# Kernel tuning notes

Measured on AMD Instinct MI355X. Metric: run time of the kernel, lower is better.

Reference implementation:

```python
import jax, jax.numpy as jnp
import numpy as np

N_POINTS = 100000
N_PAIRS = 50000   # pairs per kernel offset
K_OFFSETS = 27    # 3^3 kernel offsets for 3D kernel_size=3
C = 128


def setup_inputs() -> dict:
    key = jax.random.key(0)
    ks = jax.random.split(key, 7)
    features = jax.random.normal(ks[0], (N_POINTS, C), dtype=jnp.float32)
    in_map = jax.random.randint(ks[1], (K_OFFSETS, N_PAIRS), 0, N_POINTS)
    out_map = jax.random.randint(ks[2], (K_OFFSETS, N_PAIRS), 0, N_POINTS)
    # scale weights so two stacked convs stay numerically tame in fp32
    W0 = jax.random.normal(ks[3], (K_OFFSETS, C, C), dtype=jnp.float32) * 0.05
    b0 = jax.random.normal(ks[4], (C,), dtype=jnp.float32)
    W1 = jax.random.normal(ks[5], (K_OFFSETS, C, C), dtype=jnp.float32) * 0.05
    b1 = jax.random.normal(ks[6], (C,), dtype=jnp.float32)
    return {"features": features, "in_map": in_map, "out_map": out_map,
            "W0": W0, "b0": b0, "W1": W1, "b1": b1}


def _sparse_conv(x, W, b, in_map, out_map, n_out):
    """Minkowski-style sparse conv: gather -> per-offset matmul -> scatter-add.
    x: [N, C], W: [K, C, C], in_map/out_map: [K, P]."""
    gathered = x[in_map]                                  # [K, P, C]
    msg = jnp.einsum('kpc,kcd->kpd', gathered, W)         # [K, P, C]
    y = jax.ops.segment_sum(msg.reshape(-1, msg.shape[-1]),
                            out_map.reshape(-1),
                            num_segments=n_out)           # [N, C]
    return y + b


def reference(features, in_map, out_map, W0, b0, W1, b1):
    n = features.shape[0]
    out = jax.nn.relu(_sparse_conv(features, W0, b0, in_map, out_map, n))
    out = _sparse_conv(out, W1, b1, in_map, out_map, n)
    return out + features
```

## Files before the change

kernel.cpp:

```cpp
#include <hip/hip_runtime.h>

#define N_POINTS 100000
#define N_PAIRS  50000
#define K_OFFSETS 27
#define C 128
#define WPAD 136
#define CAP 48

#define CSR_GROUPS 8
#define CSR_BPG 128

typedef __attribute__((ext_vector_type(8))) short short8;
typedef __attribute__((ext_vector_type(4))) float floatx4;

__device__ inline unsigned short f2bf(float f) {
  unsigned int u = __float_as_uint(f);
  return (unsigned short)((u + 0x7FFFu + ((u >> 16) & 1u)) >> 16);
}
__device__ inline float bf2f(unsigned int lo16) {
  return __uint_as_float(lo16 << 16);
}

__global__ __launch_bounds__(256) void prep_w_kernel(
    const float* __restrict__ W0, const float* __restrict__ W1,
    unsigned short* __restrict__ WT0, unsigned short* __restrict__ WT1) {
  int i = blockIdx.x * 256 + threadIdx.x;
  const int per = K_OFFSETS * C * C;
  if (i >= 2 * per) return;
  const float* W = (i < per) ? W0 : W1;
  unsigned short* WT = (i < per) ? WT0 : WT1;
  int r = (i < per) ? i : i - per;
  int k = r / (C * C);
  int q = r % (C * C);
  int d = q / C;
  int c = q % C;
  WT[k * C * C + d * C + c] = f2bf(W[k * C * C + c * C + d]);
}

__global__ __launch_bounds__(256) void prep_x_kernel(
    const float* __restrict__ features, const float* __restrict__ b0,
    unsigned short* __restrict__ xb, float* __restrict__ out, int write_out) {
  int i = (blockIdx.x * 256 + threadIdx.x) * 4;
  if (i >= N_POINTS * C) return;
  float4 f = *(const float4*)&features[i];
  ushort4 u;
  u.x = f2bf(f.x); u.y = f2bf(f.y); u.z = f2bf(f.z); u.w = f2bf(f.w);
  *(ushort4*)&xb[i] = u;
  if (write_out) {
    float4 b = *(const float4*)&b0[i & 127];
    *(float4*)&out[i] = b;
  }
}

__global__ __launch_bounds__(256) void zero_counts_kernel(int* __restrict__ counts) {
  int i = blockIdx.x * 256 + threadIdx.x;
  if (i < N_POINTS) counts[i] = 0;
}

__global__ __launch_bounds__(256) void build_csr_kernel(
    const int* __restrict__ out_map, int* __restrict__ counts, int* __restrict__ idxbuf) {
  const int grp = blockIdx.x & (CSR_GROUPS - 1);
  const int blk = blockIdx.x >> 3;
  const int lo = grp * (N_POINTS / CSR_GROUPS);
  const int hi = lo + (N_POINTS / CSR_GROUPS);
  const int total4 = K_OFFSETS * N_PAIRS / 4;
  for (int i4 = blk * 256 + (int)threadIdx.x; i4 < total4; i4 += CSR_BPG * 256) {
    int4 o4 = *(const int4*)&out_map[i4 * 4];
    int o[4] = {o4.x, o4.y, o4.z, o4.w};
#pragma unroll
    for (int j = 0; j < 4; ++j) {
      if (o[j] >= lo && o[j] < hi) {
        int pos = atomicAdd(&counts[o[j]], 1);
        int flat = i4 * 4 + j;
        int k = flat / N_PAIRS;
        int p = flat - k * N_PAIRS;
        if (pos < CAP) idxbuf[o[j] * CAP + pos] = (k << 16) | p;
      }
    }
  }
}

__global__ __launch_bounds__(256, 4) void conv_msg_kernel(
    const unsigned short* __restrict__ xb, const unsigned short* __restrict__ wbt,
    const int* __restrict__ in_map, unsigned short* __restrict__ msg, int k0) {
  __shared__ unsigned short Wlds[C * WPAD];

  const int k = k0 + blockIdx.y;
  const int pairBase = blockIdx.x * 128;
  const int tid = threadIdx.x;

  const unsigned short* wk = wbt + k * C * C;
#pragma unroll
  for (int it = 0; it < 8; ++it) {
    int t = tid + it * 256;
    int row = t >> 4;
    int col = (t & 15) << 3;
    *(uint4*)&Wlds[row * WPAD + col] = *(const uint4*)&wk[row * C + col];
  }
  __syncthreads();

  const int wave = tid >> 6;
  const int lane = tid & 63;
  const int l15 = lane & 15;
  const int kg = lane >> 4;
  const int pair0 = pairBase + wave * 32;

  const int prA0 = pair0 + l15;
  const int prA1 = pair0 + 16 + l15;
  const int inIdx0 = (prA0 < N_PAIRS) ? in_map[k * N_PAIRS + prA0] : 0;
  const int inIdx1 = (prA1 < N_PAIRS) ? in_map[k * N_PAIRS + prA1] : 0;
  const unsigned short* arow0 = xb + (size_t)inIdx0 * C + kg * 8;
  const unsigned short* arow1 = xb + (size_t)inIdx1 * C + kg * 8;

  floatx4 acc0[8], acc1[8];
#pragma unroll
  for (int nt = 0; nt < 8; ++nt) {
    acc0[nt] = (floatx4){0.f, 0.f, 0.f, 0.f};
    acc1[nt] = (floatx4){0.f, 0.f, 0.f, 0.f};
  }

#pragma unroll
  for (int kk = 0; kk < 4; ++kk) {
    short8 a0 = *(const short8*)(arow0 + kk * 32);
    short8 a1 = *(const short8*)(arow1 + kk * 32);
    const unsigned short* bbase = &Wlds[l15 * WPAD + kk * 32 + kg * 8];
#pragma unroll
    for (int nt = 0; nt < 8; ++nt) {
      short8 b = *(const short8*)(bbase + nt * 16 * WPAD);
      acc0[nt] = __builtin_amdgcn_mfma_f32_16x16x32_bf16(a0, b, acc0[nt], 0, 0, 0);
      acc1[nt] = __builtin_amdgcn_mfma_f32_16x16x32_bf16(a1, b, acc1[nt], 0, 0, 0);
    }
  }

#pragma unroll
  for (int i = 0; i < 4; ++i) {
    int pr0 = pair0 + kg * 4 + i;
    if (pr0 < N_PAIRS) {
      unsigned short* row = msg + (size_t)(blockIdx.y * N_PAIRS + pr0) * C;
      uint4 v;
      v.x = (unsigned int)f2bf(acc0[0][i]) | ((unsigned int)f2bf(acc0[1][i]) << 16);
      v.y = (unsigned int)f2bf(acc0[2][i]) | ((unsigned int)f2bf(acc0[3][i]) << 16);
      v.z = (unsigned int)f2bf(acc0[4][i]) | ((unsigned int)f2bf(acc0[5][i]) << 16);
      v.w = (unsigned int)f2bf(acc0[6][i]) | ((unsigned int)f2bf(acc0[7][i]) << 16);
      *(uint4*)(row + l15 * 8) = v;
    }
    int pr1 = pair0 + 16 + kg * 4 + i;
    if (pr1 < N_PAIRS) {
      unsigned short* row = msg + (size_t)(blockIdx.y * N_PAIRS + pr1) * C;
      uint4 v;
      v.x = (unsigned int)f2bf(acc1[0][i]) | ((unsigned int)f2bf(acc1[1][i]) << 16);
      v.y = (unsigned int)f2bf(acc1[2][i]) | ((unsigned int)f2bf(acc1[3][i]) << 16);
      v.z = (unsigned int)f2bf(acc1[4][i]) | ((unsigned int)f2bf(acc1[5][i]) << 16);
      v.w = (unsigned int)f2bf(acc1[6][i]) | ((unsigned int)f2bf(acc1[7][i]) << 16);
      *(uint4*)(row + l15 * 8) = v;
    }
  }
}

__global__ __launch_bounds__(256) void gather_kernel(
    const unsigned short* __restrict__ msg, const int* __restrict__ counts,
    const int* __restrict__ idxbuf, const float* __restrict__ bias,
    const float* __restrict__ features, float* __restrict__ out,
    unsigned short* __restrict__ x1b,
    int k0, int G, int init_mode, int fin_mode) {
  __shared__ int elds[4][64];
  const int wave = threadIdx.x >> 6;
  const int lane = threadIdx.x & 63;
  const int oi = blockIdx.x * 4 + wave;

  const int c0 = ((2 * lane) & 7) * 16 + (lane >> 2);
  const int c1 = c0 + 16;
  const size_t base = (size_t)oi * C;

  float a0, a1;
  if (init_mode == 1)      { a0 = bias[c0]; a1 = bias[c1]; }
  else if (init_mode == 2) { a0 = bias[c0] + features[base + c0];
                             a1 = bias[c1] + features[base + c1]; }
  else                     { a0 = out[base + c0]; a1 = out[base + c1]; }

  int cnt = counts[oi]; if (cnt > CAP) cnt = CAP;

  int e_mine = (lane < cnt) ? idxbuf[oi * CAP + lane] : 0;
  bool ok = false;
  if (lane < cnt) {
    unsigned int rel = ((unsigned int)e_mine >> 16) - (unsigned int)k0;
    ok = rel < (unsigned int)G;
  }
  unsigned long long mask = __ballot(ok);
  int cnt2 = __popcll(mask);
  if (ok) {
    int pos = __popcll(mask & ((1ull << lane) - 1ull));
    unsigned int rel = ((unsigned int)e_mine >> 16) - (unsigned int)k0;
    elds[wave][pos] = (int)(rel * N_PAIRS + ((unsigned int)e_mine & 0xffffu));
  }
  __syncthreads();

  const unsigned short* mbase = msg + 2 * lane;
  int t = 0;
  for (; t + 4 <= cnt2; t += 4) {
    int f0 = elds[wave][t];
    int f1 = elds[wave][t + 1];
    int f2 = elds[wave][t + 2];
    int f3 = elds[wave][t + 3];
    unsigned int v0 = *(const unsigned int*)(mbase + (size_t)f0 * C);
    unsigned int v1 = *(const unsigned int*)(mbase + (size_t)f1 * C);
    unsigned int v2 = *(const unsigned int*)(mbase + (size_t)f2 * C);
    unsigned int v3 = *(const unsigned int*)(mbase + (size_t)f3 * C);
    a0 += bf2f(v0 & 0xffffu) + bf2f(v1 & 0xffffu) + bf2f(v2 & 0xffffu) + bf2f(v3 & 0xffffu);
    a1 += bf2f(v0 >> 16) + bf2f(v1 >> 16) + bf2f(v2 >> 16) + bf2f(v3 >> 16);
  }
  for (; t < cnt2; ++t) {
    int f0 = elds[wave][t];
    unsigned int v = *(const unsigned int*)(mbase + (size_t)f0 * C);
    a0 += bf2f(v & 0xffffu);
    a1 += bf2f(v >> 16);
  }

  if (fin_mode == 1) {
    x1b[base + c0] = f2bf(fmaxf(a0, 0.f));
    x1b[base + c1] = f2bf(fmaxf(a1, 0.f));
  } else {
    out[base + c0] = a0;
    out[base + c1] = a1;
  }
}

__global__ __launch_bounds__(256) void mid_kernel(
    const float* __restrict__ features, const float* __restrict__ b1,
    float* __restrict__ out, unsigned short* __restrict__ x1b) {
  int i = (blockIdx.x * 256 + threadIdx.x) * 4;
  if (i >= N_POINTS * C) return;
  float4 y = *(const float4*)&out[i];
  ushort4 u;
  u.x = f2bf(fmaxf(y.x, 0.f));
  u.y = f2bf(fmaxf(y.y, 0.f));
  u.z = f2bf(fmaxf(y.z, 0.f));
  u.w = f2bf(fmaxf(y.w, 0.f));
  *(ushort4*)&x1b[i] = u;
  float4 f = *(const float4*)&features[i];
  float4 b = *(const float4*)&b1[i & 127];
  float4 o;
  o.x = f.x + b.x; o.y = f.y + b.y; o.z = f.z + b.z; o.w = f.w + b.w;
  *(float4*)&out[i] = o;
}

__global__ __launch_bounds__(256, 4) void conv_atomic_kernel(
    const unsigned short* __restrict__ xb, const unsigned short* __restrict__ wbt,
    const int* __restrict__ in_map, const int* __restrict__ out_map,
    float* __restrict__ out) {
  __shared__ unsigned short Wlds[C * WPAD];
  const int k = blockIdx.y;
  const int pairBase = blockIdx.x * 64;
  const int tid = threadIdx.x;
  const unsigned short* wk = wbt + k * C * C;
#pragma unroll
  for (int it = 0; it < 8; ++it) {
    int t = tid + it * 256;
    int row = t >> 4;
    int col = (t & 15) << 3;
    *(uint4*)&Wlds[row * WPAD + col] = *(const uint4*)&wk[row * C + col];
  }
  __syncthreads();
  const int wave = tid >> 6;
  const int lane = tid & 63;
  const int l15 = lane & 15;
  const int kg = lane >> 4;
  const int pair0 = pairBase + wave * 16;
  const int prA = pair0 + l15;
  const int inIdx = (prA < N_PAIRS) ? in_map[k * N_PAIRS + prA] : 0;
  const unsigned short* arow = xb + (size_t)inIdx * C + kg * 8;
  floatx4 acc[8];
#pragma unroll
  for (int nt = 0; nt < 8; ++nt) acc[nt] = (floatx4){0.f, 0.f, 0.f, 0.f};
#pragma unroll
  for (int kk = 0; kk < 4; ++kk) {
    short8 a = *(const short8*)(arow + kk * 32);
    const unsigned short* bbase = &Wlds[l15 * WPAD + kk * 32 + kg * 8];
#pragma unroll
    for (int nt = 0; nt < 8; ++nt) {
      short8 b = *(const short8*)(bbase + nt * 16 * WPAD);
      acc[nt] = __builtin_amdgcn_mfma_f32_16x16x32_bf16(a, b, acc[nt], 0, 0, 0);
    }
  }
#pragma unroll
  for (int i = 0; i < 4; ++i) {
    int pr = pair0 + kg * 4 + i;
    if (pr < N_PAIRS) {
      int oi = out_map[k * N_PAIRS + pr];
      float* orow = out + (size_t)oi * C + l15;
#pragma unroll
      for (int nt = 0; nt < 8; ++nt) atomicAdd(orow + nt * 16, acc[nt][i]);
    }
  }
}

extern "C" void kernel_launch(void* const* d_in, const int* in_sizes, int n_in,
                              void* d_out, int out_size, void* d_ws, size_t ws_size,
                              hipStream_t stream) {
  const float* features = (const float*)d_in[0];
  const int* in_map     = (const int*)d_in[1];
  const int* out_map    = (const int*)d_in[2];
  const float* W0       = (const float*)d_in[3];
  const float* b0       = (const float*)d_in[4];
  const float* W1       = (const float*)d_in[5];
  const float* b1       = (const float*)d_in[6];
  float* out = (float*)d_out;

  char* ws = (char*)d_ws;
  unsigned short* xb  = (unsigned short*)(ws);
  unsigned short* x1b = (unsigned short*)(ws + 25600000);
  unsigned short* WT0 = (unsigned short*)(ws + 51200000);
  unsigned short* WT1 = (unsigned short*)(ws + 52084736);
  int* counts         = (int*)(ws + 52969472);
  int* idxbuf         = (int*)(ws + 53369856);
  unsigned short* msg = (unsigned short*)(ws + 72569856);

  const long long MSG_K_BYTES = (long long)N_PAIRS * C * 2;
  long long avail = (long long)ws_size - 72569856LL;
  int G = 0;
  if (avail >= MSG_K_BYTES) {
    long long g = avail / MSG_K_BYTES;
    G = (int)(g > K_OFFSETS ? K_OFFSETS : g);
  }

  prep_w_kernel<<<(2 * K_OFFSETS * C * C + 255) / 256, 256, 0, stream>>>(W0, W1, WT0, WT1);
  prep_x_kernel<<<(N_POINTS * C / 4 + 255) / 256, 256, 0, stream>>>(
      features, b0, xb, out, (G > 0) ? 0 : 1);

  if (G > 0) {
    zero_counts_kernel<<<(N_POINTS + 255) / 256, 256, 0, stream>>>(counts);
    build_csr_kernel<<<CSR_GROUPS * CSR_BPG, 256, 0, stream>>>(out_map, counts, idxbuf);

    const int nchunks = (K_OFFSETS + G - 1) / G;
    for (int layer = 0; layer < 2; ++layer) {
      const unsigned short* xin = layer ? x1b : xb;
      const unsigned short* wt  = layer ? WT1 : WT0;
      const float* bias         = layer ? b1  : b0;
      for (int c = 0; c < nchunks; ++c) {
        int k0 = c * G;
        int Gc = K_OFFSETS - k0 < G ? K_OFFSETS - k0 : G;
        dim3 cgrid((N_PAIRS + 127) / 128, Gc);
        conv_msg_kernel<<<cgrid, 256, 0, stream>>>(xin, wt, in_map, msg, k0);
        int init_mode = (c == 0) ? (layer ? 2 : 1) : 0;
        int fin_mode  = (layer == 0 && c == nchunks - 1) ? 1 : 0;
        gather_kernel<<<N_POINTS / 4, 256, 0, stream>>>(
            msg, counts, idxbuf, bias, features, out, x1b, k0, Gc, init_mode, fin_mode);
      }
    }
  } else {
    dim3 cgrid((N_PAIRS + 63) / 64, K_OFFSETS);
    conv_atomic_kernel<<<cgrid, 256, 0, stream>>>(xb, WT0, in_map, out_map, out);
    mid_kernel<<<(N_POINTS * C / 4 + 255) / 256, 256, 0, stream>>>(features, b1, out, x1b);
    conv_atomic_kernel<<<cgrid, 256, 0, stream>>>(x1b, WT1, in_map, out_map, out);
  }
}
```

Baseline: 672.7 us.

## Write messages into per-output CSR slots so gather reads contiguous rows

Replaces the capped per-output index list with a counting pass plus prefix-sum allocation per chunk. The conv kernel now claims a slot by atomic cursor and writes each message row directly into the output point's contiguous segment. The gather then streams consecutive rows without index lookups, LDS compaction or a barrier. This removes the CAP truncation but adds an atomic and an out_map read per pair row in the conv kernel, and the scattered writes may hurt store coalescing.

```diff
diff --git a/kernel.cpp b/kernel.cpp
--- a/kernel.cpp
+++ b/kernel.cpp
@@ -5,7 +5,8 @@
 #define K_OFFSETS 27
 #define C 128
 #define WPAD 136
-#define CAP 48
+
+#define NCH_MAX 7
 
 #define CSR_GROUPS 8
 #define CSR_BPG 128
@@ -52,13 +53,15 @@
   }
 }
 
-__global__ __launch_bounds__(256) void zero_counts_kernel(int* __restrict__ counts) {
+__global__ __launch_bounds__(256) void zero_meta_kernel(
+    int* __restrict__ countc, int* __restrict__ ccur) {
   int i = blockIdx.x * 256 + threadIdx.x;
-  if (i < N_POINTS) counts[i] = 0;
-}
-
-__global__ __launch_bounds__(256) void build_csr_kernel(
-    const int* __restrict__ out_map, int* __restrict__ counts, int* __restrict__ idxbuf) {
+  if (i < NCH_MAX * N_POINTS) countc[i] = 0;
+  if (i < NCH_MAX) ccur[i] = 0;
+}
+
+__global__ __launch_bounds__(256) void count_kernel(
+    const int* __restrict__ out_map, int* __restrict__ countc, int PG) {
   const int grp = blockIdx.x & (CSR_GROUPS - 1);
   const int blk = blockIdx.x >> 3;
   const int lo = grp * (N_POINTS / CSR_GROUPS);
@@ -70,19 +73,42 @@
 #pragma unroll
     for (int j = 0; j < 4; ++j) {
       if (o[j] >= lo && o[j] < hi) {
-        int pos = atomicAdd(&counts[o[j]], 1);
-        int flat = i4 * 4 + j;
-        int k = flat / N_PAIRS;
-        int p = flat - k * N_PAIRS;
-        if (pos < CAP) idxbuf[o[j] * CAP + pos] = (k << 16) | p;
+        int c = (i4 * 4 + j) / PG;
+        atomicAdd(&countc[c * N_POINTS + o[j]], 1);
       }
     }
   }
 }
 
-__global__ __launch_bounds__(256, 4) void conv_msg_kernel(
+__global__ __launch_bounds__(256) void alloc_kernel(
+    const int* __restrict__ countc, int* __restrict__ startc,
+    int* __restrict__ cursA, int* __restrict__ cursB, int* __restrict__ ccur) {
+  const int c = blockIdx.y;
+  const int oi = blockIdx.x * 256 + (int)threadIdx.x;
+  const int lane = threadIdx.x & 63;
+  int cnt = (oi < N_POINTS) ? countc[c * N_POINTS + oi] : 0;
+  int x = cnt;
+#pragma unroll
+  for (int off = 1; off < 64; off <<= 1) {
+    int y = __shfl_up(x, off);
+    if (lane >= off) x += y;
+  }
+  int wtot = __shfl(x, 63);
+  int base = 0;
+  if (lane == 63) base = atomicAdd(&ccur[c], wtot);
+  base = __shfl(base, 63);
+  int s = base + x - cnt;
+  if (oi < N_POINTS) {
+    startc[c * N_POINTS + oi] = s;
+    cursA[c * N_POINTS + oi] = s;
+    cursB[c * N_POINTS + oi] = s;
+  }
+}
+
+__global__ __launch_bounds__(256, 4) void conv_msg_csr_kernel(
     const unsigned short* __restrict__ xb, const unsigned short* __restrict__ wbt,
-    const int* __restrict__ in_map, unsigned short* __restrict__ msg, int k0) {
+    const int* __restrict__ in_map, const int* __restrict__ out_map,
+    int* __restrict__ curs, unsigned short* __restrict__ msg2, int k0) {
   __shared__ unsigned short Wlds[C * WPAD];
 
   const int k = k0 + blockIdx.y;
@@ -136,7 +162,11 @@
   for (int i = 0; i < 4; ++i) {
     int pr0 = pair0 + kg * 4 + i;
     if (pr0 < N_PAIRS) {
-      unsigned short* row = msg + (size_t)(blockIdx.y * N_PAIRS + pr0) * C;
+      int o = out_map[k * N_PAIRS + pr0];
+      int sl = 0;
+      if (l15 == 0) sl = atomicAdd(&curs[o], 1);
+      sl = __shfl(sl, kg * 16);
+      unsigned short* row = msg2 + (size_t)sl * C;
       uint4 v;
       v.x = (unsigned int)f2bf(acc0[0][i]) | ((unsigned int)f2bf(acc0[1][i]) << 16);
       v.y = (unsigned int)f2bf(acc0[2][i]) | ((unsigned int)f2bf(acc0[3][i]) << 16);
@@ -146,7 +176,11 @@
     }
     int pr1 = pair0 + 16 + kg * 4 + i;
     if (pr1 < N_PAIRS) {
-      unsigned short* row = msg + (size_t)(blockIdx.y * N_PAIRS + pr1) * C;
+      int o = out_map[k * N_PAIRS + pr1];
+      int sl = 0;
+      if (l15 == 0) sl = atomicAdd(&curs[o], 1);
+      sl = __shfl(sl, kg * 16);
+      unsigned short* row = msg2 + (size_t)sl * C;
       uint4 v;
       v.x = (unsigned int)f2bf(acc1[0][i]) | ((unsigned int)f2bf(acc1[1][i]) << 16);
       v.y = (unsigned int)f2bf(acc1[2][i]) | ((unsigned int)f2bf(acc1[3][i]) << 16);
@@ -157,13 +191,11 @@
   }
 }
 
-__global__ __launch_bounds__(256) void gather_kernel(
-    const unsigned short* __restrict__ msg, const int* __restrict__ counts,
-    const int* __restrict__ idxbuf, const float* __restrict__ bias,
+__global__ __launch_bounds__(256) void gather_csr_kernel(
+    const unsigned short* __restrict__ msg2, const int* __restrict__ countc,
+    const int* __restrict__ startc, const float* __restrict__ bias,
     const float* __restrict__ features, float* __restrict__ out,
-    unsigned short* __restrict__ x1b,
-    int k0, int G, int init_mode, int fin_mode) {
-  __shared__ int elds[4][64];
+    unsigned short* __restrict__ x1b, int init_mode, int fin_mode) {
   const int wave = threadIdx.x >> 6;
   const int lane = threadIdx.x & 63;
   const int oi = blockIdx.x * 4 + wave;
@@ -178,40 +210,21 @@
                              a1 = bias[c1] + features[base + c1]; }
   else                     { a0 = out[base + c0]; a1 = out[base + c1]; }
 
-  int cnt = counts[oi]; if (cnt > CAP) cnt = CAP;
-
-  int e_mine = (lane < cnt) ? idxbuf[oi * CAP + lane] : 0;
-  bool ok = false;
-  if (lane < cnt) {
-    unsigned int rel = ((unsigned int)e_mine >> 16) - (unsigned int)k0;
-    ok = rel < (unsigned int)G;
-  }
-  unsigned long long mask = __ballot(ok);
-  int cnt2 = __popcll(mask);
-  if (ok) {
-    int pos = __popcll(mask & ((1ull << lane) - 1ull));
-    unsigned int rel = ((unsigned int)e_mine >> 16) - (unsigned int)k0;
-    elds[wave][pos] = (int)(rel * N_PAIRS + ((unsigned int)e_mine & 0xffffu));
-  }
-  __syncthreads();
-
-  const unsigned short* mbase = msg + 2 * lane;
+  const int cnt = countc[oi];
+  const int s0 = startc[oi];
+  const unsigned short* mb = msg2 + (size_t)s0 * C + 2 * lane;
+
   int t = 0;
-  for (; t + 4 <= cnt2; t += 4) {
-    int f0 = elds[wave][t];
-    int f1 = elds[wave][t + 1];
-    int f2 = elds[wave][t + 2];
-    int f3 = elds[wave][t + 3];
-    unsigned int v0 = *(const unsigned int*)(mbase + (size_t)f0 * C);
-    unsigned int v1 = *(const unsigned int*)(mbase + (size_t)f1 * C);
-    unsigned int v2 = *(const unsigned int*)(mbase + (size_t)f2 * C);
-    unsigned int v3 = *(const unsigned int*)(mbase + (size_t)f3 * C);
+  for (; t + 4 <= cnt; t += 4) {
+    unsigned int v0 = *(const unsigned int*)(mb + (t + 0) * C);
+    unsigned int v1 = *(const unsigned int*)(mb + (t + 1) * C);
+    unsigned int v2 = *(const unsigned int*)(mb + (t + 2) * C);
+    unsigned int v3 = *(const unsigned int*)(mb + (t + 3) * C);
     a0 += bf2f(v0 & 0xffffu) + bf2f(v1 & 0xffffu) + bf2f(v2 & 0xffffu) + bf2f(v3 & 0xffffu);
     a1 += bf2f(v0 >> 16) + bf2f(v1 >> 16) + bf2f(v2 >> 16) + bf2f(v3 >> 16);
   }
-  for (; t < cnt2; ++t) {
-    int f0 = elds[wave][t];
-    unsigned int v = *(const unsigned int*)(mbase + (size_t)f0 * C);
+  for (; t < cnt; ++t) {
+    unsigned int v = *(const unsigned int*)(mb + t * C);
     a0 += bf2f(v & 0xffffu);
     a1 += bf2f(v >> 16);
   }
@@ -311,40 +324,51 @@
   unsigned short* x1b = (unsigned short*)(ws + 25600000);
   unsigned short* WT0 = (unsigned short*)(ws + 51200000);
   unsigned short* WT1 = (unsigned short*)(ws + 52084736);
-  int* counts         = (int*)(ws + 52969472);
-  int* idxbuf         = (int*)(ws + 53369856);
-  unsigned short* msg = (unsigned short*)(ws + 72569856);
+  int* countc         = (int*)(ws + 52969472);
+  int* startc         = (int*)(ws + 55769472);
+  int* cursA          = (int*)(ws + 58569472);
+  int* cursB          = (int*)(ws + 61369472);
+  int* ccur           = (int*)(ws + 64169472);
+  unsigned short* msg2 = (unsigned short*)(ws + 64169600);
 
   const long long MSG_K_BYTES = (long long)N_PAIRS * C * 2;
-  long long avail = (long long)ws_size - 72569856LL;
+  long long avail = (long long)ws_size - 64169600LL;
   int G = 0;
   if (avail >= MSG_K_BYTES) {
     long long g = avail / MSG_K_BYTES;
     G = (int)(g > K_OFFSETS ? K_OFFSETS : g);
   }
+  int nchunks = (G > 0) ? (K_OFFSETS + G - 1) / G : 0;
+  const int use_fused = (G > 0 && nchunks <= NCH_MAX) ? 1 : 0;
 
   prep_w_kernel<<<(2 * K_OFFSETS * C * C + 255) / 256, 256, 0, stream>>>(W0, W1, WT0, WT1);
   prep_x_kernel<<<(N_POINTS * C / 4 + 255) / 256, 256, 0, stream>>>(
-      features, b0, xb, out, (G > 0) ? 0 : 1);
-
-  if (G > 0) {
-    zero_counts_kernel<<<(N_POINTS + 255) / 256, 256, 0, stream>>>(counts);
-    build_csr_kernel<<<CSR_GROUPS * CSR_BPG, 256, 0, stream>>>(out_map, counts, idxbuf);
-
-    const int nchunks = (K_OFFSETS + G - 1) / G;
+      features, b0, xb, out, use_fused ? 0 : 1);
+
+  if (use_fused) {
+    zero_meta_kernel<<<(NCH_MAX * N_POINTS + 255) / 256, 256, 0, stream>>>(countc, ccur);
+    count_kernel<<<CSR_GROUPS * CSR_BPG, 256, 0, stream>>>(out_map, countc, N_PAIRS * G);
+    {
+      dim3 agrid((N_POINTS + 255) / 256, nchunks);
+      alloc_kernel<<<agrid, 256, 0, stream>>>(countc, startc, cursA, cursB, ccur);
+    }
+
     for (int layer = 0; layer < 2; ++layer) {
       const unsigned short* xin = layer ? x1b : xb;
       const unsigned short* wt  = layer ? WT1 : WT0;
       const float* bias         = layer ? b1  : b0;
+      int* curs                 = layer ? cursB : cursA;
       for (int c = 0; c < nchunks; ++c) {
         int k0 = c * G;
         int Gc = K_OFFSETS - k0 < G ? K_OFFSETS - k0 : G;
         dim3 cgrid((N_PAIRS + 127) / 128, Gc);
-        conv_msg_kernel<<<cgrid, 256, 0, stream>>>(xin, wt, in_map, msg, k0);
+        conv_msg_csr_kernel<<<cgrid, 256, 0, stream>>>(
+            xin, wt, in_map, out_map, curs + (size_t)c * N_POINTS, msg2, k0);
         int init_mode = (c == 0) ? (layer ? 2 : 1) : 0;
         int fin_mode  = (layer == 0 && c == nchunks - 1) ? 1 : 0;
-        gather_kernel<<<N_POINTS / 4, 256, 0, stream>>>(
-            msg, counts, idxbuf, bias, features, out, x1b, k0, Gc, init_mode, fin_mode);
+        gather_csr_kernel<<<N_POINTS / 4, 256, 0, stream>>>(
+            msg2, countc + (size_t)c * N_POINTS, startc + (size_t)c * N_POINTS,
+            bias, features, out, x1b, init_mode, fin_mode);
       }
     }
   } else {
```

Measured after the change: 817.3 us. 1.21x slower.

## Partition pairs by output quarter so message buffer fits cache-sized chunks

Applied to the files above, without the earlier changes.

Pairs are bucketed by output-point quarter and kernel offset into a compact pairlist, and the CSR now stores direct slot indices into a per-quarter message buffer. Each layer runs conv and gather four times, once per quarter. The per-quarter message buffer (about 90 MB) replaces the full per-offset buffer, which is meant to improve cache reuse in the gather and to remove the ballot and filtering work. The cost is extra preprocessing passes (histogram, scan, two-pass build), more kernel launches, and conv blocks that exit early on padding.

```diff
diff --git a/kernel.cpp b/kernel.cpp
--- a/kernel.cpp
+++ b/kernel.cpp
@@ -6,6 +6,11 @@
 #define C 128
 #define WPAD 136
 #define CAP 48
+
+#define NQ 4
+#define QPTS 25000
+#define MSGCAP 360448
+#define GX 110
 
 #define CSR_GROUPS 8
 #define CSR_BPG 128
@@ -52,41 +57,103 @@
   }
 }
 
-__global__ __launch_bounds__(256) void zero_counts_kernel(int* __restrict__ counts) {
+__global__ __launch_bounds__(256) void zero_meta_kernel(
+    int* __restrict__ counts, int* __restrict__ counts_hk) {
   int i = blockIdx.x * 256 + threadIdx.x;
   if (i < N_POINTS) counts[i] = 0;
-}
-
-__global__ __launch_bounds__(256) void build_csr_kernel(
-    const int* __restrict__ out_map, int* __restrict__ counts, int* __restrict__ idxbuf) {
+  if (i < NQ * K_OFFSETS) counts_hk[i] = 0;
+}
+
+__global__ __launch_bounds__(256) void count_hk_kernel(
+    const int* __restrict__ out_map, int* __restrict__ counts_hk) {
+  __shared__ int hist[NQ * K_OFFSETS];
+  if (threadIdx.x < NQ * K_OFFSETS) hist[threadIdx.x] = 0;
+  __syncthreads();
+  const int total4 = K_OFFSETS * N_PAIRS / 4;
+  for (int i4 = blockIdx.x * 256 + (int)threadIdx.x; i4 < total4; i4 += 256 * 256) {
+    int4 o4 = *(const int4*)&out_map[i4 * 4];
+    int o[4] = {o4.x, o4.y, o4.z, o4.w};
+    int k = (i4 * 4) / N_PAIRS;
+#pragma unroll
+    for (int j = 0; j < 4; ++j) atomicAdd(&hist[(o[j] / QPTS) * K_OFFSETS + k], 1);
+  }
+  __syncthreads();
+  if (threadIdx.x < NQ * K_OFFSETS)
+    atomicAdd(&counts_hk[threadIdx.x], hist[threadIdx.x]);
+}
+
+__global__ void scan_kernel(const int* __restrict__ counts_hk,
+                            int* __restrict__ base_hk, int* __restrict__ cursor_hk) {
+  if (threadIdx.x < NQ) {
+    int h = threadIdx.x;
+    int run = 0;
+    for (int k = 0; k < K_OFFSETS; ++k) {
+      base_hk[h * K_OFFSETS + k] = run;
+      cursor_hk[h * K_OFFSETS + k] = run;
+      run += (counts_hk[h * K_OFFSETS + k] + 31) & ~31;
+    }
+  }
+}
+
+__global__ __launch_bounds__(256) void build2_kernel(
+    const int* __restrict__ out_map, const int* __restrict__ in_map,
+    int* __restrict__ counts, int* __restrict__ idxbuf,
+    int* __restrict__ cursor_hk, int* __restrict__ pairlist) {
+  __shared__ int histA[K_OFFSETS];
+  __shared__ int kbase[K_OFFSETS];
   const int grp = blockIdx.x & (CSR_GROUPS - 1);
   const int blk = blockIdx.x >> 3;
+  const int h = grp >> 1;
   const int lo = grp * (N_POINTS / CSR_GROUPS);
   const int hi = lo + (N_POINTS / CSR_GROUPS);
+  if (threadIdx.x < K_OFFSETS) histA[threadIdx.x] = 0;
+  __syncthreads();
   const int total4 = K_OFFSETS * N_PAIRS / 4;
   for (int i4 = blk * 256 + (int)threadIdx.x; i4 < total4; i4 += CSR_BPG * 256) {
     int4 o4 = *(const int4*)&out_map[i4 * 4];
     int o[4] = {o4.x, o4.y, o4.z, o4.w};
+    int k = (i4 * 4) / N_PAIRS;
+#pragma unroll
+    for (int j = 0; j < 4; ++j)
+      if (o[j] >= lo && o[j] < hi) atomicAdd(&histA[k], 1);
+  }
+  __syncthreads();
+  if (threadIdx.x < K_OFFSETS) {
+    kbase[threadIdx.x] =
+        atomicAdd(&cursor_hk[h * K_OFFSETS + threadIdx.x], histA[threadIdx.x]);
+    histA[threadIdx.x] = 0;
+  }
+  __syncthreads();
+  for (int i4 = blk * 256 + (int)threadIdx.x; i4 < total4; i4 += CSR_BPG * 256) {
+    int4 o4 = *(const int4*)&out_map[i4 * 4];
+    int4 n4 = *(const int4*)&in_map[i4 * 4];
+    int o[4] = {o4.x, o4.y, o4.z, o4.w};
+    int n[4] = {n4.x, n4.y, n4.z, n4.w};
+    int k = (i4 * 4) / N_PAIRS;
 #pragma unroll
     for (int j = 0; j < 4; ++j) {
       if (o[j] >= lo && o[j] < hi) {
+        int pk = atomicAdd(&histA[k], 1);
+        int slot = kbase[k] + pk;
+        pairlist[h * MSGCAP + slot] = n[j];
         int pos = atomicAdd(&counts[o[j]], 1);
-        int flat = i4 * 4 + j;
-        int k = flat / N_PAIRS;
-        int p = flat - k * N_PAIRS;
-        if (pos < CAP) idxbuf[o[j] * CAP + pos] = (k << 16) | p;
+        if (pos < CAP) idxbuf[o[j] * CAP + pos] = slot;
       }
     }
   }
 }
 
-__global__ __launch_bounds__(256, 4) void conv_msg_kernel(
-    const unsigned short* __restrict__ xb, const unsigned short* __restrict__ wbt,
-    const int* __restrict__ in_map, unsigned short* __restrict__ msg, int k0) {
+__global__ __launch_bounds__(256, 4) void conv2_kernel(
+    const unsigned short* __restrict__ xin, const unsigned short* __restrict__ wbt,
+    const int* __restrict__ counts_hk, const int* __restrict__ base_hk,
+    const int* __restrict__ pairlist, unsigned short* __restrict__ msg2, int h) {
   __shared__ unsigned short Wlds[C * WPAD];
-
-  const int k = k0 + blockIdx.y;
-  const int pairBase = blockIdx.x * 128;
+  const int k = blockIdx.y;
+  const int cnt = counts_hk[h * K_OFFSETS + k];
+  const int cpad = (cnt + 31) & ~31;
+  const int off0 = blockIdx.x * 128;
+  if (off0 >= cpad) return;
+  const int kb = base_hk[h * K_OFFSETS + k];
   const int tid = threadIdx.x;
 
   const unsigned short* wk = wbt + k * C * C;
@@ -103,14 +170,15 @@
   const int lane = tid & 63;
   const int l15 = lane & 15;
   const int kg = lane >> 4;
-  const int pair0 = pairBase + wave * 32;
-
-  const int prA0 = pair0 + l15;
-  const int prA1 = pair0 + 16 + l15;
-  const int inIdx0 = (prA0 < N_PAIRS) ? in_map[k * N_PAIRS + prA0] : 0;
-  const int inIdx1 = (prA1 < N_PAIRS) ? in_map[k * N_PAIRS + prA1] : 0;
-  const unsigned short* arow0 = xb + (size_t)inIdx0 * C + kg * 8;
-  const unsigned short* arow1 = xb + (size_t)inIdx1 * C + kg * 8;
+  const int ws0 = off0 + wave * 32;
+  if (ws0 >= cpad) return;
+
+  const int s0 = kb + ws0;
+  const int plbase = h * MSGCAP;
+  const int n0 = pairlist[plbase + s0 + l15] & 0x1FFFF;
+  const int n1 = pairlist[plbase + s0 + 16 + l15] & 0x1FFFF;
+  const unsigned short* arow0 = xin + (size_t)n0 * C + kg * 8;
+  const unsigned short* arow1 = xin + (size_t)n1 * C + kg * 8;
 
   floatx4 acc0[8], acc1[8];
 #pragma unroll
@@ -118,7 +186,6 @@
     acc0[nt] = (floatx4){0.f, 0.f, 0.f, 0.f};
     acc1[nt] = (floatx4){0.f, 0.f, 0.f, 0.f};
   }
-
 #pragma unroll
   for (int kk = 0; kk < 4; ++kk) {
     short8 a0 = *(const short8*)(arow0 + kk * 32);
@@ -131,12 +198,10 @@
       acc1[nt] = __builtin_amdgcn_mfma_f32_16x16x32_bf16(a1, b, acc1[nt], 0, 0, 0);
     }
   }
-
 #pragma unroll
   for (int i = 0; i < 4; ++i) {
-    int pr0 = pair0 + kg * 4 + i;
-    if (pr0 < N_PAIRS) {
-      unsigned short* row = msg + (size_t)(blockIdx.y * N_PAIRS + pr0) * C;
+    {
+      unsigned short* row = msg2 + (size_t)(s0 + kg * 4 + i) * C;
       uint4 v;
       v.x = (unsigned int)f2bf(acc0[0][i]) | ((unsigned int)f2bf(acc0[1][i]) << 16);
       v.y = (unsigned int)f2bf(acc0[2][i]) | ((unsigned int)f2bf(acc0[3][i]) << 16);
@@ -144,9 +209,8 @@
       v.w = (unsigned int)f2bf(acc0[6][i]) | ((unsigned int)f2bf(acc0[7][i]) << 16);
       *(uint4*)(row + l15 * 8) = v;
     }
-    int pr1 = pair0 + 16 + kg * 4 + i;
-    if (pr1 < N_PAIRS) {
-      unsigned short* row = msg + (size_t)(blockIdx.y * N_PAIRS + pr1) * C;
+    {
+      unsigned short* row = msg2 + (size_t)(s0 + 16 + kg * 4 + i) * C;
       uint4 v;
       v.x = (unsigned int)f2bf(acc1[0][i]) | ((unsigned int)f2bf(acc1[1][i]) << 16);
       v.y = (unsigned int)f2bf(acc1[2][i]) | ((unsigned int)f2bf(acc1[3][i]) << 16);
@@ -157,66 +221,51 @@
   }
 }
 
-__global__ __launch_bounds__(256) void gather_kernel(
-    const unsigned short* __restrict__ msg, const int* __restrict__ counts,
+__global__ __launch_bounds__(256) void gather2_kernel(
+    const unsigned short* __restrict__ msg2, const int* __restrict__ counts,
     const int* __restrict__ idxbuf, const float* __restrict__ bias,
     const float* __restrict__ features, float* __restrict__ out,
-    unsigned short* __restrict__ x1b,
-    int k0, int G, int init_mode, int fin_mode) {
+    unsigned short* __restrict__ x1b, int h, int layer) {
   __shared__ int elds[4][64];
   const int wave = threadIdx.x >> 6;
   const int lane = threadIdx.x & 63;
-  const int oi = blockIdx.x * 4 + wave;
+  const int oi = h * QPTS + blockIdx.x * 4 + wave;
 
   const int c0 = ((2 * lane) & 7) * 16 + (lane >> 2);
   const int c1 = c0 + 16;
   const size_t base = (size_t)oi * C;
 
   float a0, a1;
-  if (init_mode == 1)      { a0 = bias[c0]; a1 = bias[c1]; }
-  else if (init_mode == 2) { a0 = bias[c0] + features[base + c0];
-                             a1 = bias[c1] + features[base + c1]; }
-  else                     { a0 = out[base + c0]; a1 = out[base + c1]; }
+  if (layer == 0) { a0 = bias[c0]; a1 = bias[c1]; }
+  else            { a0 = bias[c0] + features[base + c0];
+                    a1 = bias[c1] + features[base + c1]; }
 
   int cnt = counts[oi]; if (cnt > CAP) cnt = CAP;
-
-  int e_mine = (lane < cnt) ? idxbuf[oi * CAP + lane] : 0;
-  bool ok = false;
-  if (lane < cnt) {
-    unsigned int rel = ((unsigned int)e_mine >> 16) - (unsigned int)k0;
-    ok = rel < (unsigned int)G;
-  }
-  unsigned long long mask = __ballot(ok);
-  int cnt2 = __popcll(mask);
-  if (ok) {
-    int pos = __popcll(mask & ((1ull << lane) - 1ull));
-    unsigned int rel = ((unsigned int)e_mine >> 16) - (unsigned int)k0;
-    elds[wave][pos] = (int)(rel * N_PAIRS + ((unsigned int)e_mine & 0xffffu));
-  }
-  __syncthreads();
-
-  const unsigned short* mbase = msg + 2 * lane;
+  if (lane < cnt) elds[wave][lane] = idxbuf[oi * CAP + lane];
+  __syncthreads();
+
+  const unsigned short* mb = msg2 + 2 * lane;
   int t = 0;
-  for (; t + 4 <= cnt2; t += 4) {
+  for (; t + 4 <= cnt; t += 4) {
     int f0 = elds[wave][t];
     int f1 = elds[wave][t + 1];
     int f2 = elds[wave][t + 2];
     int f3 = elds[wave][t + 3];
-    unsigned int v0 = *(const unsigned int*)(mbase + (size_t)f0 * C);
-    unsigned int v1 = *(const unsigned int*)(mbase + (size_t)f1 * C);
-    unsigned int v2 = *(const unsigned int*)(mbase + (size_t)f2 * C);
-    unsigned int v3 = *(const unsigned int*)(mbase + (size_t)f3 * C);
+    unsigned int v0 = *(const unsigned int*)(mb + (size_t)f0 * C);
+    unsigned int v1 = *(const unsigned int*)(mb + (size_t)f1 * C);
+    unsigned int v2 = *(const unsigned int*)(mb + (size_t)f2 * C);
+    unsigned int v3 = *(const unsigned int*)(mb + (size_t)f3 * C);
     a0 += bf2f(v0 & 0xffffu) + bf2f(v1 & 0xffffu) + bf2f(v2 & 0xffffu) + bf2f(v3 & 0xffffu);
     a1 += bf2f(v0 >> 16) + bf2f(v1 >> 16) + bf2f(v2 >> 16) + bf2f(v3 >> 16);
   }
-  for (; t < cnt2; ++t) {
+  for (; t < cnt; ++t) {
     int f0 = elds[wave][t];
-    unsigned int v = *(const unsigned int*)(mbase + (size_t)f0 * C);
+    unsigned int v = *(const unsigned int*)(mb + (size_t)f0 * C);
     a0 += bf2f(v & 0xffffu);
     a1 += bf2f(v >> 16);
   }
 
-  if (fin_mode == 1) {
+  if (layer == 0) {
     x1b[base + c0] = f2bf(fmaxf(a0, 0.f));
     x1b[base + c1] = f2bf(fmaxf(a1, 0.f));
   } else {
@@ -312,39 +361,36 @@
   unsigned short* WT0 = (unsigned short*)(ws + 51200000);
   unsigned short* WT1 = (unsigned short*)(ws + 52084736);
   int* counts         = (int*)(ws + 52969472);
-  int* idxbuf         = (int*)(ws + 53369856);
-  unsigned short* msg = (unsigned short*)(ws + 72569856);
-
-  const long long MSG_K_BYTES = (long long)N_PAIRS * C * 2;
-  long long avail = (long long)ws_size - 72569856LL;
-  int G = 0;
-  if (avail >= MSG_K_BYTES) {
-    long long g = avail / MSG_K_BYTES;
-    G = (int)(g > K_OFFSETS ? K_OFFSETS : g);
-  }
+  int* counts_hk      = (int*)(ws + 53369856);
+  int* base_hk        = (int*)(ws + 53370368);
+  int* cursor_hk      = (int*)(ws + 53370880);
+  int* pairlist       = (int*)(ws + 53371392);
+  int* idxbuf         = (int*)(ws + 59138560);
+  unsigned short* msg2 = (unsigned short*)(ws + 78338560);
+
+  const int use2 = (ws_size >= 170613248ULL) ? 1 : 0;
 
   prep_w_kernel<<<(2 * K_OFFSETS * C * C + 255) / 256, 256, 0, stream>>>(W0, W1, WT0, WT1);
   prep_x_kernel<<<(N_POINTS * C / 4 + 255) / 256, 256, 0, stream>>>(
-      features, b0, xb, out, (G > 0) ? 0 : 1);
-
-  if (G > 0) {
-    zero_counts_kernel<<<(N_POINTS + 255) / 256, 256, 0, stream>>>(counts);
-    build_csr_kernel<<<CSR_GROUPS * CSR_BPG, 256, 0, stream>>>(out_map, counts, idxbuf);
-
-    const int nchunks = (K_OFFSETS + G - 1) / G;
+      features, b0, xb, out, use2 ? 0 : 1);
+
+  if (use2) {
+    zero_meta_kernel<<<(N_POINTS + 255) / 256, 256, 0, stream>>>(counts, counts_hk);
+    count_hk_kernel<<<256, 256, 0, stream>>>(out_map, counts_hk);
+    scan_kernel<<<1, 64, 0, stream>>>(counts_hk, base_hk, cursor_hk);
+    build2_kernel<<<CSR_GROUPS * CSR_BPG, 256, 0, stream>>>(
+        out_map, in_map, counts, idxbuf, cursor_hk, pairlist);
+
     for (int layer = 0; layer < 2; ++layer) {
       const unsigned short* xin = layer ? x1b : xb;
       const unsigned short* wt  = layer ? WT1 : WT0;
       const float* bias         = layer ? b1  : b0;
-      for (int c = 0; c < nchunks; ++c) {
-        int k0 = c * G;
-        int Gc = K_OFFSETS - k0 < G ? K_OFFSETS - k0 : G;
-        dim3 cgrid((N_PAIRS + 127) / 128, Gc);
-        conv_msg_kernel<<<cgrid, 256, 0, stream>>>(xin, wt, in_map, msg, k0);
-        int init_mode = (c == 0) ? (layer ? 2 : 1) : 0;
-        int fin_mode  = (layer == 0 && c == nchunks - 1) ? 1 : 0;
-        gather_kernel<<<N_POINTS / 4, 256, 0, stream>>>(
-            msg, counts, idxbuf, bias, features, out, x1b, k0, Gc, init_mode, fin_mode);
+      for (int h = 0; h < NQ; ++h) {
+        dim3 cgrid(GX, K_OFFSETS);
+        conv2_kernel<<<cgrid, 256, 0, stream>>>(
+            xin, wt, counts_hk, base_hk, pairlist, msg2, h);
+        gather2_kernel<<<QPTS / 4, 256, 0, stream>>>(
+            msg2, counts, idxbuf, bias, features, out, x1b, h, layer);
       }
     }
   } else {
```

Result: no change. 671.6 us (-0.2%).
